# Kernel optimization log

Hardware: AMD Instinct MI355X
Metric: run time of the kernel (lower is better)

## Reference

```python
import jax, jax.numpy as jnp
import numpy as np
from jax import lax

B, T, IN, H, OUT, OC = 64, 1024, 128, 512, 128, 64


def setup_inputs() -> dict:
    key = jax.random.key(0)
    ks = jax.random.split(key, 9)
    s = 0.05
    return {
        "inX": jax.random.normal(ks[0], (B, T, IN), jnp.float32),
        "r": jnp.zeros((1,), jnp.float32),
        "conv_w": jax.random.normal(ks[1], (OC, IN, 3), jnp.float32) * s,
        "conv_b": jax.random.normal(ks[2], (OC,), jnp.float32) * s,
        "w_ih": jax.random.normal(ks[3], (4 * H, OC), jnp.float32) * s,
        "w_hh": jax.random.normal(ks[4], (4 * H, H), jnp.float32) * s,
        "b_ih": jax.random.normal(ks[5], (4 * H,), jnp.float32) * s,
        "b_hh": jax.random.normal(ks[6], (4 * H,), jnp.float32) * s,
        "lin_w": jax.random.normal(ks[7], (OUT, H), jnp.float32) * s,
        "lin_b": jax.random.normal(ks[8], (OUT,), jnp.float32) * s,
        "batch_size": B,
    }


def reference(inX, r, conv_w, conv_b, w_ih, w_hh, b_ih, b_hh, lin_w, lin_b, batch_size):
    # F.normalize along dim=2 (L2, eps=1e-12)
    nrm = jnp.sqrt(jnp.sum(inX * inX, axis=2, keepdims=True))
    x = inX / jnp.maximum(nrm, 1e-12)
    # [B, C, L] conv1d, valid padding, stride 1
    x = x.transpose(0, 2, 1)
    y = lax.conv_general_dilated(x, conv_w, (1,), "VALID",
                                 dimension_numbers=("NCH", "OIH", "NCH"))
    y = jax.nn.relu(y + conv_b[None, :, None])
    seq = y.transpose(2, 0, 1)  # [T', B, OC]

    h0 = jnp.zeros((batch_size, w_hh.shape[1]), inX.dtype)
    c0 = jnp.zeros_like(h0)

    def step(carry, xt):
        h, c = carry
        gates = xt @ w_ih.T + b_ih + h @ w_hh.T + b_hh
        i, f, g, o = jnp.split(gates, 4, axis=-1)
        c = jax.nn.sigmoid(f) * c + jax.nn.sigmoid(i) * jnp.tanh(g)
        h = jax.nn.sigmoid(o) * jnp.tanh(c)
        return (h, c), None

    (h, c), _ = lax.scan(step, (h0, c0), seq)
    return h @ lin_w.T + lin_b
```

## Files before the change

### kernel.cpp

```cpp
#include <hip/hip_runtime.h>

typedef __attribute__((ext_vector_type(8))) short short8;
typedef __attribute__((ext_vector_type(4))) float f32x4;
typedef unsigned short u16;
typedef unsigned long long u64;

#define TP   1022
#define NWRK 32

#define OFF_WPACK   0
#define OFF_SEQ     2359296
#define OFF_BIAS    10993664
#define OFF_H0      11001856
#define OFF_H1      11067392
#define OFF_HFIN    11132928
#define OFF_BAR     11264000

__device__ inline u16 f2bf(float x) {
  union { float f; unsigned u; } un; un.f = x;
  unsigned r = un.u + 0x7fffu + ((un.u >> 16) & 1u);
  return (u16)(r >> 16);
}
__device__ inline float sigmoidf_(float x) { return 1.f / (1.f + __expf(-x)); }
__device__ inline float tanhf_(float x)    { return 2.f / (1.f + __expf(-2.f * x)) - 1.f; }

__device__ inline f32x4 load16_sc0(const void* p) {
  f32x4 r;
  asm volatile("global_load_dwordx4 %0, %1, off sc0" : "=v"(r) : "v"(p) : "memory");
  return r;
}
__device__ inline void store16_sc0(void* p, f32x4 v) {
  asm volatile("global_store_dwordx4 %0, %1, off sc0" :: "v"(p), "v"(v) : "memory");
}

__global__ void k_init(const float* __restrict__ b_ih, const float* __restrict__ b_hh,
                       float* __restrict__ biasp, unsigned* __restrict__ hzero,
                       unsigned* __restrict__ bar) {
  int tid = blockIdx.x * 256 + threadIdx.x;
  if (tid < 32768) hzero[tid] = 0u;
  if (tid < 2048) {
    int j = tid >> 2, g = tid & 3;
    int row = g * 512 + j;
    biasp[tid] = b_ih[row] + b_hh[row];
  }
  if (tid < 128) bar[tid] = 0u;
}

__global__ void k_pack(const float* __restrict__ w_ih, const float* __restrict__ w_hh,
                       u16* __restrict__ wp) {
  int idx = blockIdx.x * 256 + threadIdx.x;
  int nt = idx / 9216;
  int rem = idx - nt * 9216;
  int kt = rem / 512;
  int rem2 = rem - kt * 512;
  int lane = rem2 >> 3, i = rem2 & 7;
  int n = nt * 16 + (lane & 15);
  int k = kt * 32 + (lane >> 4) * 8 + i;
  int j = n >> 2, g = n & 3;
  int row = g * 512 + j;
  float v = (k < 64) ? w_ih[row * 64 + k] : w_hh[row * 512 + (k - 64)];
  wp[idx] = f2bf(v);
}

__global__ __launch_bounds__(256) void k_conv(const float* __restrict__ inX,
                                              const float* __restrict__ conv_w,
                                              const float* __restrict__ conv_b,
                                              u16* __restrict__ seq) {
  __shared__ float xn[6][128];
  __shared__ float rn[6];
  int b = blockIdx.y;
  int t0 = blockIdx.x * 4;
  int tid = threadIdx.x;
  for (int e = tid; e < 768; e += 256) {
    int ri = e >> 7, col = e & 127;
    int t = t0 + ri;
    xn[ri][col] = (t < 1024) ? inX[((size_t)b * 1024 + t) * 128 + col] : 0.f;
  }
  __syncthreads();
  if (tid < 192) {
    int ri = tid >> 5, l32 = tid & 31;
    float4 v = *reinterpret_cast<const float4*>(&xn[ri][l32 * 4]);
    float s = v.x * v.x + v.y * v.y + v.z * v.z + v.w * v.w;
    #pragma unroll
    for (int d = 1; d < 32; d <<= 1) s += __shfl_xor(s, d, 32);
    if (l32 == 0) rn[ri] = 1.f / fmaxf(sqrtf(s), 1e-12f);
  }
  __syncthreads();
  for (int e = tid; e < 768; e += 256) {
    int ri = e >> 7, col = e & 127;
    xn[ri][col] *= rn[ri];
  }
  __syncthreads();
  int oc = tid & 63, ty = tid >> 6;
  int t = t0 + ty;
  if (t < TP) {
    const float* wr = conv_w + oc * 384;
    float s = conv_b[oc];
    #pragma unroll 4
    for (int i = 0; i < 128; ++i) {
      s += wr[i * 3 + 0] * xn[ty + 0][i]
         + wr[i * 3 + 1] * xn[ty + 1][i]
         + wr[i * 3 + 2] * xn[ty + 2][i];
    }
    s = fmaxf(s, 0.f);
    seq[((size_t)t * 64 + b) * 64 + oc] = f2bf(s);
  }
}

__global__ __launch_bounds__(256, 1) void k_lstm(const u16* __restrict__ seq,
                                                 const u16* __restrict__ wp,
                                                 const float* __restrict__ biasp,
                                                 u16* h0buf, u16* h1buf,
                                                 float* __restrict__ hfin,
                                                 unsigned* bar) {
  const int tid = threadIdx.x;
  __shared__ int s_rank;
  __shared__ __align__(16) char hl[32768];
  __shared__ u16 ostage[32][40];

  if (tid == 0) {
    unsigned xcd;
    asm volatile("s_getreg_b32 %0, hwreg(HW_REG_XCC_ID)" : "=s"(xcd));
    xcd &= 7u;
    unsigned r = __hip_atomic_fetch_add(&bar[8 + xcd], 1u, __ATOMIC_RELAXED,
                                        __HIP_MEMORY_SCOPE_AGENT);
    if (r == NWRK - 1) {
      unsigned expected = 0u;
      __hip_atomic_compare_exchange_strong(&bar[16], &expected, xcd + 1u,
                                           __ATOMIC_RELAXED, __ATOMIC_RELAXED,
                                           __HIP_MEMORY_SCOPE_AGENT);
    }
    unsigned d;
    while ((d = __hip_atomic_load(&bar[16], __ATOMIC_RELAXED,
                                  __HIP_MEMORY_SCOPE_AGENT)) == 0u)
      __builtin_amdgcn_s_sleep(8);
    s_rank = (xcd == d - 1u && r < NWRK) ? (int)r : -1;
  }
  __syncthreads();
  const int rank = s_rank;

  if (rank < 0) {
    const int lane_ = tid & 63;
    float x = (float)tid + 1.0f;
    unsigned d = 0;
    do {
      #pragma unroll
      for (int i = 0; i < 1024; ++i) x = __builtin_fmaf(x, 1.0000001f, 1.0e-30f);
      asm volatile("" :: "v"(x));
      if (lane_ == 0)
        d = __hip_atomic_fetch_add(&bar[64], 0u, __ATOMIC_RELAXED,
                                   __HIP_MEMORY_SCOPE_AGENT);
      d = __shfl(d, 0);
    } while (d < NWRK);
    return;
  }

  const int wave = tid >> 6, lane = tid & 63;
  const int g   = rank >> 4;
  const int wgi = rank & 15;
  const int B0  = g * 32;
  const int U0  = wgi * 32;
  const int mt2 = wgi * 4 + wave;
  const int mtA = 2 * mt2, mtB = mtA + 1;
  const int bl  = lane & 15;
  const int bA  = B0 + bl;
  const int hi  = lane >> 4;
  const int koff = hi * 8;
  const int ulA = 8 * wave + hi;
  const int ulB = ulA + 4;
  const int uA  = U0 + ulA;
  const int uB  = U0 + ulB;
  const float4 biasA = *reinterpret_cast<const float4*>(biasp + mtA * 16 + hi * 4);
  const float4 biasB = *reinterpret_cast<const float4*>(biasp + mtB * 16 + hi * 4);

  short8 wA[18], wB[18];
  {
    const u16* wa = wp + (size_t)mtA * (18 * 512) + lane * 8;
    const u16* wb = wp + (size_t)mtB * (18 * 512) + lane * 8;
    #pragma unroll
    for (int kt = 0; kt < 18; ++kt) {
      wA[kt] = *reinterpret_cast<const short8*>(wa + kt * 512);
      wB[kt] = *reinterpret_cast<const short8*>(wb + kt * 512);
    }
  }

  unsigned* cnt = bar;
  float cA0 = 0.f, cA1 = 0.f, cB0 = 0.f, cB1 = 0.f;
  f32x4 accA0, accA1, accB0, accB1;

  const int r0base = bl * 1024;
  const int r1base = r0base + 16 * 1024;
  const int rmask  = (bl & 7) << 4;
  const int fr_hib = hi * 16;

#define XPART(T) do { \
    const u16* xt_ = seq + (size_t)(T) * 4096; \
    short8 x0a = *reinterpret_cast<const short8*>(xt_ + bA * 64 + koff); \
    short8 x1a = *reinterpret_cast<const short8*>(xt_ + (bA + 16) * 64 + koff); \
    short8 x0b = *reinterpret_cast<const short8*>(xt_ + bA * 64 + 32 + koff); \
    short8 x1b = *reinterpret_cast<const short8*>(xt_ + (bA + 16) * 64 + 32 + koff); \
    f32x4 z_ = {0.f, 0.f, 0.f, 0.f}; \
    accA0 = __builtin_amdgcn_mfma_f32_16x16x32_bf16(wA[0], x0a, z_, 0, 0, 0); \
    accA1 = __builtin_amdgcn_mfma_f32_16x16x32_bf16(wA[0], x1a, z_, 0, 0, 0); \
    accB0 = __builtin_amdgcn_mfma_f32_16x16x32_bf16(wB[0], x0a, z_, 0, 0, 0); \
    accB1 = __builtin_amdgcn_mfma_f32_16x16x32_bf16(wB[0], x1a, z_, 0, 0, 0); \
    accA0 = __builtin_amdgcn_mfma_f32_16x16x32_bf16(wA[1], x0b, accA0, 0, 0, 0); \
    accA1 = __builtin_amdgcn_mfma_f32_16x16x32_bf16(wA[1], x1b, accA1, 0, 0, 0); \
    accB0 = __builtin_amdgcn_mfma_f32_16x16x32_bf16(wB[1], x0b, accB0, 0, 0, 0); \
    accB1 = __builtin_amdgcn_mfma_f32_16x16x32_bf16(wB[1], x1b, accB1, 0, 0, 0); \
  } while (0)

  XPART(0);

  for (int t = 0; t < TP; ++t) {
    if (t > 0) {
      if (tid == 0) {
        const unsigned tgt = (unsigned)(NWRK * t);
        for (;;) {
          unsigned v = __hip_atomic_fetch_add(cnt, 0u, __ATOMIC_RELAXED,
                                              __HIP_MEMORY_SCOPE_WORKGROUP);
          if (v >= tgt) break;
          __builtin_amdgcn_s_sleep(1);
        }
      }
      __syncthreads();
    }

    const u16* hc = (t & 1) ? h1buf : h0buf;
    u16* hn = (t & 1) ? h0buf : h1buf;

    {
      const u16* hsrc = hc + (size_t)B0 * 512;
      f32x4 va[4], vb[4];
      #pragma unroll
      for (int p = 0; p < 4; ++p)
        va[p] = load16_sc0(hsrc + (size_t)(p * 256 + tid) * 8);
      #pragma unroll
      for (int p = 0; p < 4; ++p)
        vb[p] = load16_sc0(hsrc + (size_t)((p + 4) * 256 + tid) * 8);
      asm volatile("s_waitcnt vmcnt(4)" ::: "memory");
      __builtin_amdgcn_sched_barrier(0);
      #pragma unroll
      for (int p = 0; p < 4; ++p) {
        int chunk = p * 256 + tid;
        int row = chunk >> 6, off = (chunk & 63) * 16;
        *reinterpret_cast<f32x4*>(hl + row * 1024 + (off ^ ((row & 7) << 4))) = va[p];
      }
      asm volatile("s_waitcnt vmcnt(0)" ::: "memory");
      __builtin_amdgcn_sched_barrier(0);
      #pragma unroll
      for (int p = 0; p < 4; ++p) {
        int chunk = (p + 4) * 256 + tid;
        int row = chunk >> 6, off = (chunk & 63) * 16;
        *reinterpret_cast<f32x4*>(hl + row * 1024 + (off ^ ((row & 7) << 4))) = vb[p];
      }
    }
    __syncthreads();

    #pragma unroll
    for (int kt = 0; kt < 16; ++kt) {
      int off = (kt * 64 + fr_hib) ^ rmask;
      short8 b0 = *reinterpret_cast<const short8*>(hl + r0base + off);
      short8 b1 = *reinterpret_cast<const short8*>(hl + r1base + off);
      accA0 = __builtin_amdgcn_mfma_f32_16x16x32_bf16(wA[kt + 2], b0, accA0, 0, 0, 0);
      accA1 = __builtin_amdgcn_mfma_f32_16x16x32_bf16(wA[kt + 2], b1, accA1, 0, 0, 0);
      accB0 = __builtin_amdgcn_mfma_f32_16x16x32_bf16(wB[kt + 2], b0, accB0, 0, 0, 0);
      accB1 = __builtin_amdgcn_mfma_f32_16x16x32_bf16(wB[kt + 2], b1, accB1, 0, 0, 0);
    }

    float iA0 = sigmoidf_(accA0[0] + biasA.x);
    float fA0 = sigmoidf_(accA0[1] + biasA.y);
    float gA0 = tanhf_(accA0[2] + biasA.z);
    float oA0 = sigmoidf_(accA0[3] + biasA.w);
    cA0 = fA0 * cA0 + iA0 * gA0;
    float hvA0 = oA0 * tanhf_(cA0);
    float iA1 = sigmoidf_(accA1[0] + biasA.x);
    float fA1 = sigmoidf_(accA1[1] + biasA.y);
    float gA1 = tanhf_(accA1[2] + biasA.z);
    float oA1 = sigmoidf_(accA1[3] + biasA.w);
    cA1 = fA1 * cA1 + iA1 * gA1;
    float hvA1 = oA1 * tanhf_(cA1);
    float iB0 = sigmoidf_(accB0[0] + biasB.x);
    float fB0 = sigmoidf_(accB0[1] + biasB.y);
    float gB0 = tanhf_(accB0[2] + biasB.z);
    float oB0 = sigmoidf_(accB0[3] + biasB.w);
    cB0 = fB0 * cB0 + iB0 * gB0;
    float hvB0 = oB0 * tanhf_(cB0);
    float iB1 = sigmoidf_(accB1[0] + biasB.x);
    float fB1 = sigmoidf_(accB1[1] + biasB.y);
    float gB1 = tanhf_(accB1[2] + biasB.z);
    float oB1 = sigmoidf_(accB1[3] + biasB.w);
    cB1 = fB1 * cB1 + iB1 * gB1;
    float hvB1 = oB1 * tanhf_(cB1);

    ostage[bl][ulA]      = f2bf(hvA0);
    ostage[bl + 16][ulA] = f2bf(hvA1);
    ostage[bl][ulB]      = f2bf(hvB0);
    ostage[bl + 16][ulB] = f2bf(hvB1);
    if (t == TP - 1) {
      hfin[bA * 512 + uA]        = hvA0;
      hfin[(bA + 16) * 512 + uA] = hvA1;
      hfin[bA * 512 + uB]        = hvB0;
      hfin[(bA + 16) * 512 + uB] = hvB1;
    }
    __syncthreads();

    if (tid < 128) {
      int b_l = tid >> 2, q = tid & 3;
      f32x4 val = *reinterpret_cast<const f32x4*>(&ostage[b_l][q * 8]);
      store16_sc0(hn + (size_t)(B0 + b_l) * 512 + U0 + q * 8, val);
    }
    asm volatile("s_waitcnt vmcnt(0)" ::: "memory");
    __syncthreads();

    if (tid == 0)
      __hip_atomic_fetch_add(cnt, 1u, __ATOMIC_RELAXED, __HIP_MEMORY_SCOPE_WORKGROUP);

    if (t + 1 < TP) XPART(t + 1);
  }
#undef XPART

  if (tid == 0)
    __hip_atomic_fetch_add(&bar[64], 1u, __ATOMIC_RELAXED, __HIP_MEMORY_SCOPE_AGENT);
}

__global__ void k_fc(const float* __restrict__ hfin, const float* __restrict__ lin_w,
                     const float* __restrict__ lin_b, float* __restrict__ out) {
  int b = blockIdx.x, o = threadIdx.x;
  const float* hp = hfin + b * 512;
  const float* wq = lin_w + o * 512;
  float s = lin_b[o];
  #pragma unroll 4
  for (int j = 0; j < 512; ++j) s += hp[j] * wq[j];
  out[b * 128 + o] = s;
}

extern "C" void kernel_launch(void* const* d_in, const int* in_sizes, int n_in,
                              void* d_out, int out_size, void* d_ws, size_t ws_size,
                              hipStream_t stream) {
  const float* inX    = (const float*)d_in[0];
  const float* conv_w = (const float*)d_in[2];
  const float* conv_b = (const float*)d_in[3];
  const float* w_ih   = (const float*)d_in[4];
  const float* w_hh   = (const float*)d_in[5];
  const float* b_ih   = (const float*)d_in[6];
  const float* b_hh   = (const float*)d_in[7];
  const float* lin_w  = (const float*)d_in[8];
  const float* lin_b  = (const float*)d_in[9];
  float* out = (float*)d_out;
  char* ws = (char*)d_ws;
  u16*      wpack = (u16*)(ws + OFF_WPACK);
  u16*      seq   = (u16*)(ws + OFF_SEQ);
  float*    biasp = (float*)(ws + OFF_BIAS);
  u16*      h0b   = (u16*)(ws + OFF_H0);
  u16*      h1b   = (u16*)(ws + OFF_H1);
  float*    hfin  = (float*)(ws + OFF_HFIN);
  unsigned* bar   = (unsigned*)(ws + OFF_BAR);

  k_init<<<dim3(128), dim3(256), 0, stream>>>(b_ih, b_hh, biasp, (unsigned*)(ws + OFF_H0), bar);
  k_pack<<<dim3(4608), dim3(256), 0, stream>>>(w_ih, w_hh, wpack);
  k_conv<<<dim3(256, 64), dim3(256), 0, stream>>>(inX, conv_w, conv_b, seq);
  k_lstm<<<dim3(256), dim3(256), 0, stream>>>(seq, wpack, biasp, h0b, h1b, hfin, bar);
  k_fc<<<dim3(64), dim3(128), 0, stream>>>(hfin, lin_w, lin_b, out);
}
```

Before: 3.937 ms.

## Split step barrier into per-batch-group counters and overlap h load with MFMA

The single global step counter shared by all 32 workgroups is replaced by one counter per batch group of 16 workgroups, since each group only reads the h rows of its own 32 batch entries. This removes cross-group coupling at every timestep. The h tile load is also reorganised so the first half of the K dimension is staged to LDS and consumed by MFMAs while the second half's global loads are still in flight, with an extra workgroup barrier in between. The finish counter moves to a different slot to avoid colliding with the new group counters.

```diff
diff --git a/kernel.cpp b/kernel.cpp
--- a/kernel.cpp
+++ b/kernel.cpp
@@ -148,7 +148,7 @@
       for (int i = 0; i < 1024; ++i) x = __builtin_fmaf(x, 1.0000001f, 1.0e-30f);
       asm volatile("" :: "v"(x));
       if (lane_ == 0)
-        d = __hip_atomic_fetch_add(&bar[64], 0u, __ATOMIC_RELAXED,
+        d = __hip_atomic_fetch_add(&bar[96], 0u, __ATOMIC_RELAXED,
                                    __HIP_MEMORY_SCOPE_AGENT);
       d = __shfl(d, 0);
     } while (d < NWRK);
@@ -184,7 +184,7 @@
     }
   }
 
-  unsigned* cnt = bar;
+  unsigned* grpcnt = &bar[g * 32];
   float cA0 = 0.f, cA1 = 0.f, cB0 = 0.f, cB1 = 0.f;
   f32x4 accA0, accA1, accB0, accB1;
 
@@ -192,6 +192,10 @@
   const int r1base = r0base + 16 * 1024;
   const int rmask  = (bl & 7) << 4;
   const int fr_hib = hi * 16;
+
+  const int strow = tid >> 5;
+  const int stcol = tid & 31;
+  const int stswz = strow << 4;
 
 #define XPART(T) do { \
     const u16* xt_ = seq + (size_t)(T) * 4096; \
@@ -215,9 +219,9 @@
   for (int t = 0; t < TP; ++t) {
     if (t > 0) {
       if (tid == 0) {
-        const unsigned tgt = (unsigned)(NWRK * t);
+        const unsigned tgt = (unsigned)(16 * t);
         for (;;) {
-          unsigned v = __hip_atomic_fetch_add(cnt, 0u, __ATOMIC_RELAXED,
+          unsigned v = __hip_atomic_fetch_add(grpcnt, 0u, __ATOMIC_RELAXED,
                                               __HIP_MEMORY_SCOPE_WORKGROUP);
           if (v >= tgt) break;
           __builtin_amdgcn_s_sleep(1);
@@ -229,36 +233,42 @@
     const u16* hc = (t & 1) ? h1buf : h0buf;
     u16* hn = (t & 1) ? h0buf : h1buf;
 
-    {
-      const u16* hsrc = hc + (size_t)B0 * 512;
-      f32x4 va[4], vb[4];
-      #pragma unroll
-      for (int p = 0; p < 4; ++p)
-        va[p] = load16_sc0(hsrc + (size_t)(p * 256 + tid) * 8);
-      #pragma unroll
-      for (int p = 0; p < 4; ++p)
-        vb[p] = load16_sc0(hsrc + (size_t)((p + 4) * 256 + tid) * 8);
-      asm volatile("s_waitcnt vmcnt(4)" ::: "memory");
-      __builtin_amdgcn_sched_barrier(0);
-      #pragma unroll
-      for (int p = 0; p < 4; ++p) {
-        int chunk = p * 256 + tid;
-        int row = chunk >> 6, off = (chunk & 63) * 16;
-        *reinterpret_cast<f32x4*>(hl + row * 1024 + (off ^ ((row & 7) << 4))) = va[p];
-      }
-      asm volatile("s_waitcnt vmcnt(0)" ::: "memory");
-      __builtin_amdgcn_sched_barrier(0);
-      #pragma unroll
-      for (int p = 0; p < 4; ++p) {
-        int chunk = (p + 4) * 256 + tid;
-        int row = chunk >> 6, off = (chunk & 63) * 16;
-        *reinterpret_cast<f32x4*>(hl + row * 1024 + (off ^ ((row & 7) << 4))) = vb[p];
-      }
-    }
+    const u16* hsrc = hc + (size_t)B0 * 512;
+    f32x4 va[4], vb[4];
+    #pragma unroll
+    for (int p = 0; p < 4; ++p)
+      va[p] = load16_sc0(hsrc + (size_t)(p * 8 + strow) * 512 + stcol * 8);
+    #pragma unroll
+    for (int p = 0; p < 4; ++p)
+      vb[p] = load16_sc0(hsrc + (size_t)(p * 8 + strow) * 512 + 256 + stcol * 8);
+    asm volatile("s_waitcnt vmcnt(4)" ::: "memory");
+    __builtin_amdgcn_sched_barrier(0);
+    #pragma unroll
+    for (int p = 0; p < 4; ++p)
+      *reinterpret_cast<f32x4*>(hl + (p * 8 + strow) * 1024 +
+                                ((stcol * 16) ^ stswz)) = va[p];
     __syncthreads();
 
     #pragma unroll
-    for (int kt = 0; kt < 16; ++kt) {
+    for (int kt = 0; kt < 8; ++kt) {
+      int off = (kt * 64 + fr_hib) ^ rmask;
+      short8 b0 = *reinterpret_cast<const short8*>(hl + r0base + off);
+      short8 b1 = *reinterpret_cast<const short8*>(hl + r1base + off);
+      accA0 = __builtin_amdgcn_mfma_f32_16x16x32_bf16(wA[kt + 2], b0, accA0, 0, 0, 0);
+      accA1 = __builtin_amdgcn_mfma_f32_16x16x32_bf16(wA[kt + 2], b1, accA1, 0, 0, 0);
+      accB0 = __builtin_amdgcn_mfma_f32_16x16x32_bf16(wB[kt + 2], b0, accB0, 0, 0, 0);
+      accB1 = __builtin_amdgcn_mfma_f32_16x16x32_bf16(wB[kt + 2], b1, accB1, 0, 0, 0);
+    }
+
+    asm volatile("s_waitcnt vmcnt(0)" ::: "memory");
+    __builtin_amdgcn_sched_barrier(0);
+    #pragma unroll
+    for (int p = 0; p < 4; ++p)
+      *reinterpret_cast<f32x4*>(hl + (p * 8 + strow) * 1024 + 512 +
+                                ((stcol * 16) ^ stswz)) = vb[p];
+    __syncthreads();
+    #pragma unroll
+    for (int kt = 8; kt < 16; ++kt) {
       int off = (kt * 64 + fr_hib) ^ rmask;
       short8 b0 = *reinterpret_cast<const short8*>(hl + r0base + off);
       short8 b1 = *reinterpret_cast<const short8*>(hl + r1base + off);
@@ -314,14 +324,14 @@
     __syncthreads();
 
     if (tid == 0)
-      __hip_atomic_fetch_add(cnt, 1u, __ATOMIC_RELAXED, __HIP_MEMORY_SCOPE_WORKGROUP);
+      __hip_atomic_fetch_add(grpcnt, 1u, __ATOMIC_RELAXED, __HIP_MEMORY_SCOPE_WORKGROUP);
 
     if (t + 1 < TP) XPART(t + 1);
   }
 #undef XPART
 
   if (tid == 0)
-    __hip_atomic_fetch_add(&bar[64], 1u, __ATOMIC_RELAXED, __HIP_MEMORY_SCOPE_AGENT);
+    __hip_atomic_fetch_add(&bar[96], 1u, __ATOMIC_RELAXED, __HIP_MEMORY_SCOPE_AGENT);
 }
 
 __global__ void k_fc(const float* __restrict__ hfin, const float* __restrict__ lin_w,
```

Measured after the change: 3.946 ms. No clear change (+0.2%).
